# Kernel optimization log

Hardware: AMD Instinct MI355X
Metric: run time of the kernel (lower is better)

Reference implementation:

```python
import jax, jax.numpy as jnp
import numpy as np

H = 512    # hidden size
NF = 512   # num_factor
B, S = 128, 64
D0, D1 = 1536, 2048


def setup_inputs() -> dict:
    key = jax.random.key(0)
    ks = jax.random.split(key, 14)
    stdv = 1.0 / np.sqrt(H)
    u = lambda k, shape: jax.random.uniform(k, shape, jnp.float32, -stdv, stdv)
    return {
        "x0": jax.random.normal(ks[0], (B, S, D0), jnp.float32),  # auxiliary stream (skip_info=1)
        "x1": jax.random.normal(ks[1], (B, S, D1), jnp.float32),  # main encoded stream
        # SVD_Weights for stream 0 (num_gate=2, no individual part) -> weight_fh
        "wa0": u(ks[2], (2 * H, NF)),
        "wb0": jax.random.uniform(ks[3], (NF, 1), jnp.float32, 1 - stdv, 1 + stdv),
        "wc0": u(ks[4], (NF, D0)),
        "b0": u(ks[5], (2 * H,)),
        # SVD_Weights for stream 1 (num_gate=2 shared + individual) -> weight_ih
        "wa1": u(ks[6], (2 * H, NF)),
        "wb1": jax.random.uniform(ks[7], (NF, 1), jnp.float32, 1 - stdv, 1 + stdv),
        "wc1": u(ks[8], (NF, D1)),
        "b1": u(ks[9], (2 * H,)),
        "iw1": u(ks[10], (H, D1)),
        "ib1": u(ks[11], (H,)),
        # GRU hidden-to-hidden params
        "whh": u(ks[12], (3 * H, H)),
        "bhh": u(ks[13], (3 * H,)),
    }


def _svd_weight(wa, wb, wc):
    # tag = [[1.]] (length_tag == 1)  ->  mid = wb @ tag = wb[:, 0]
    # W = wa @ diag(mid) @ wc
    return (wa * wb[:, 0][None, :]) @ wc


def reference(x0, x1, wa0, wb0, wc0, b0, wa1, wb1, wc1, b1, iw1, ib1, whh, bhh):
    bsz = x1.shape[0]
    # get_all_params for stream 1: [2H shared gates; H individual n-gate]
    w_ih = jnp.concatenate([_svd_weight(wa1, wb1, wc1), iw1], axis=0)  # [3H, D1]
    b_ih = jnp.concatenate([b1, ib1], axis=0)                          # [3H]
    # get_shared_params for stream 0: auxiliary gate contributions
    w_fh = _svd_weight(wa0, wb0, wc0)                                  # [2H, D0]

    # Precompute all input-side projections (time-parallel GEMMs)
    gi = jnp.einsum('bsd,gd->bsg', x1, w_ih) + b_ih   # [B,S,3H]
    gf = jnp.einsum('bsd,gd->bsg', x0, w_fh) + b0     # [B,S,2H]
    i_r, i_i, i_n = jnp.split(gi, 3, axis=-1)
    f_r, f_i = jnp.split(gf, 2, axis=-1)

    def step(hx, xs):
        ir, ii, inn, fr, fi = xs
        gh = hx @ whh.T + bhh
        h_r, h_i, h_n = jnp.split(gh, 3, axis=-1)
        r = jax.nn.sigmoid(ir + h_r + fr)
        z = jax.nn.sigmoid(ii + h_i + fi)
        n = jnp.tanh(inn + r * h_n)
        hy = n + z * (hx - n)
        return hy, hy

    xs = tuple(jnp.swapaxes(a, 0, 1) for a in (i_r, i_i, i_n, f_r, f_i))  # time-major
    h0 = jnp.zeros((bsz, H), x1.dtype)
    hT, out = jax.lax.scan(step, h0, xs)
    return jnp.swapaxes(out, 0, 1), hT  # ([B,S,H], [B,H])
```

## Files before the change

### kernel.cpp

```cpp
#include <hip/hip_runtime.h>

#define AS1 __attribute__((address_space(1)))
#define AS3 __attribute__((address_space(3)))

typedef __attribute__((ext_vector_type(8))) short short8;
typedef __attribute__((ext_vector_type(4))) float f32x4;

static __device__ __forceinline__ unsigned short f2bf(float f) {
    unsigned u = __builtin_bit_cast(unsigned, f);
    u += 0x7FFFu + ((u >> 16) & 1u);
    return (unsigned short)(u >> 16);
}


__global__ void cvt_bf16_kernel(const float* __restrict__ in,
                                unsigned short* __restrict__ out, int n8) {
    int i = blockIdx.x * blockDim.x + threadIdx.x;
    int stride = gridDim.x * blockDim.x;
    for (; i < n8; i += stride) {
        const float4* p = (const float4*)in + 2 * (size_t)i;
        float4 a = p[0], b = p[1];
        short8 o;
        o[0] = f2bf(a.x); o[1] = f2bf(a.y); o[2] = f2bf(a.z); o[3] = f2bf(a.w);
        o[4] = f2bf(b.x); o[5] = f2bf(b.y); o[6] = f2bf(b.z); o[7] = f2bf(b.w);
        *(short8*)(out + 8 * (size_t)i) = o;
    }
}

__global__ void wab_kernel(const float* __restrict__ wa, const float* __restrict__ wb,
                           unsigned short* __restrict__ out, int n8) {
    int i = blockIdx.x * blockDim.x + threadIdx.x;
    int stride = gridDim.x * blockDim.x;
    for (; i < n8; i += stride) {
        int base = i * 8;
        int k = base & 511;
        const float4* pa = (const float4*)(wa + base);
        const float4* pb = (const float4*)(wb + k);
        float4 a0 = pa[0], a1 = pa[1], b0 = pb[0], b1 = pb[1];
        short8 o;
        o[0] = f2bf(a0.x * b0.x); o[1] = f2bf(a0.y * b0.y);
        o[2] = f2bf(a0.z * b0.z); o[3] = f2bf(a0.w * b0.w);
        o[4] = f2bf(a1.x * b1.x); o[5] = f2bf(a1.y * b1.y);
        o[6] = f2bf(a1.z * b1.z); o[7] = f2bf(a1.w * b1.w);
        *(short8*)(out + 8 * (size_t)i) = o;
    }
}

__global__ void wcT_kernel(const float* __restrict__ wc,
                           unsigned short* __restrict__ out, int N) {
    int i = blockIdx.x * blockDim.x + threadIdx.x;
    int total = N * 512;
    int stride = gridDim.x * blockDim.x;
    for (; i < total; i += stride) {
        int n = i >> 9, k = i & 511;
        out[i] = f2bf(wc[(size_t)k * N + n]);
    }
}

__global__ void bih_kernel(const float* __restrict__ b1, const float* __restrict__ ib1,
                           float* __restrict__ out) {
    int i = blockIdx.x * blockDim.x + threadIdx.x;
    if (i < 1536) out[i] = (i < 1024) ? b1[i] : ib1[i - 1024];
}

__global__ void scan_init_kernel(unsigned short* __restrict__ hbf,
                                 unsigned* __restrict__ flags) {
    int i = blockIdx.x * blockDim.x + threadIdx.x;
    if (i < 65536) hbf[i] = 0;
    if (i < 128) flags[i] = 0;
}


template <typename OutT, bool BIAS>
__global__ __launch_bounds__(256) void gemm_nt_kernel(
    const unsigned short* __restrict__ A, const unsigned short* __restrict__ B,
    OutT* __restrict__ C, const float* __restrict__ bias, int K, int ldC) {
    __shared__ __align__(16) unsigned short As[128 * 64];
    __shared__ __align__(16) unsigned short Bs[128 * 64];
    const int tid = threadIdx.x;
    const int wave = tid >> 6, lane = tid & 63;
    const long bm = (long)blockIdx.x * 128, bn = (long)blockIdx.y * 128;
    const int wr = (wave >> 1) * 64, wc = (wave & 1) * 64;
    f32x4 acc[4][4] = {};

    const int srow = tid >> 3;
    const int scol = (tid & 7) * 8;
    const unsigned short* Ag = A + bm * K + scol;
    const unsigned short* Bg = B + bn * K + scol;

    for (int kt = 0; kt < K; kt += 64) {
        __syncthreads();
#pragma unroll
        for (int i = 0; i < 4; ++i) {
            __builtin_amdgcn_global_load_lds(
                (const AS1 void*)(Ag + (long)(i * 32 + srow) * K + kt),
                (AS3 void*)(As + i * 2048 + wave * 512), 16, 0, 0);
        }
#pragma unroll
        for (int i = 0; i < 4; ++i) {
            __builtin_amdgcn_global_load_lds(
                (const AS1 void*)(Bg + (long)(i * 32 + srow) * K + kt),
                (AS3 void*)(Bs + i * 2048 + wave * 512), 16, 0, 0);
        }
        __syncthreads();
#pragma unroll
        for (int kk = 0; kk < 2; ++kk) {
            const int ko = kk * 32 + (lane >> 4) * 8;
            short8 af[4], bfr[4];
#pragma unroll
            for (int mi = 0; mi < 4; ++mi)
                af[mi] = *(const short8*)(As + (wr + mi * 16 + (lane & 15)) * 64 + ko);
#pragma unroll
            for (int ni = 0; ni < 4; ++ni)
                bfr[ni] = *(const short8*)(Bs + (wc + ni * 16 + (lane & 15)) * 64 + ko);
#pragma unroll
            for (int mi = 0; mi < 4; ++mi)
#pragma unroll
                for (int ni = 0; ni < 4; ++ni)
                    acc[mi][ni] = __builtin_amdgcn_mfma_f32_16x16x32_bf16(
                        af[mi], bfr[ni], acc[mi][ni], 0, 0, 0);
        }
    }

    const int rbase = (lane >> 4) * 4;
    const int cbase = lane & 15;
#pragma unroll
    for (int mi = 0; mi < 4; ++mi) {
#pragma unroll
        for (int ni = 0; ni < 4; ++ni) {
            long gc = bn + wc + ni * 16 + cbase;
            float bv = BIAS ? bias[gc] : 0.f;
#pragma unroll
            for (int j = 0; j < 4; ++j) {
                long gr = bm + wr + mi * 16 + rbase + j;
                float v = acc[mi][ni][j] + bv;
                if constexpr (sizeof(OutT) == 2)
                    C[gr * ldC + gc] = (OutT)f2bf(v);
                else
                    C[gr * ldC + gc] = v;
            }
        }
    }
}


__global__ __launch_bounds__(256, 1) void gru_scan_kernel(
    unsigned short* __restrict__ hbuf,
    const unsigned short* __restrict__ whh,
    const float* __restrict__ bhh,
    const float* __restrict__ gi, const float* __restrict__ gf,
    float* __restrict__ out, float* __restrict__ hT,
    unsigned* __restrict__ flags) {
    __shared__ __align__(16) unsigned short h_lds[16 * 512];
    __shared__ __align__(16) float gis[48 * 68];
    __shared__ __align__(16) float gfs[32 * 68];

    const int tid = threadIdx.x;
    const int lane = tid & 63;
    const int wv = tid >> 6;
    const int team = blockIdx.x >> 3;
    const int member = blockIdx.x & 7;
    const int r0 = team * 16;
    const int cb = member * 64;
    const int c0 = cb + wv * 16;
    const int lrow = lane & 15;
    const int q = lane >> 4;

    short8 wf[3][16];
#pragma unroll
    for (int g = 0; g < 3; ++g)
#pragma unroll
        for (int kk = 0; kk < 16; ++kk)
            wf[g][kk] = *(const short8*)(whh + (size_t)(g * 512 + c0 + lrow) * 512 + kk * 32 + q * 8);

    const int hc = c0 + lrow;
    const float br = bhh[hc], bz = bhh[512 + hc], bn_ = bhh[1024 + hc];
    const int rb = r0 + q * 4;
    const int lc = wv * 16 + lrow;
    float hprev[4] = {0.f, 0.f, 0.f, 0.f};

    const int chunk_sub = tid >> 4;
    const int u4 = (tid & 15) * 4;
    float4 sl[5];
    auto slab_load = [&](int t) {
#pragma unroll
        for (int k = 0; k < 5; ++k) {
            int chunk = k * 16 + chunk_sub;
            const float* p;
            if (chunk < 48) {
                int bbq = chunk / 3, g = chunk - bbq * 3;
                p = gi + ((size_t)(r0 + bbq) * 64 + t) * 1536 + g * 512 + cb + u4;
            } else {
                int c2 = chunk - 48, bbq = c2 >> 1, g2 = c2 & 1;
                p = gf + ((size_t)(r0 + bbq) * 64 + t) * 1024 + g2 * 512 + cb + u4;
            }
            sl[k] = *(const float4*)p;
        }
    };
    slab_load(0);

    for (int t = 0; t < 64; ++t) {
        if (t > 0 && tid < 64) {
            const unsigned tgt = (unsigned)t;
            for (;;) {
                unsigned v = __hip_atomic_load(&flags[team * 16 + (lane & 7)],
                                               __ATOMIC_RELAXED, __HIP_MEMORY_SCOPE_AGENT);
                if (__all((int)(v >= tgt))) break;
                __builtin_amdgcn_s_sleep(1);
            }
            __builtin_amdgcn_fence(__ATOMIC_ACQUIRE, "agent");
        }
        __syncthreads();

        {
            const unsigned short* hin = hbuf + (t & 1) * 65536;
            const int srow = tid >> 4;
            const unsigned long long* hs =
                (const unsigned long long*)(hin + (size_t)(r0 + srow) * 512);
            unsigned long long hq[8];
#pragma unroll
            for (int k = 0; k < 8; ++k)
                hq[k] = __hip_atomic_load(hs + (tid & 15) + k * 16,
                                          __ATOMIC_RELAXED, __HIP_MEMORY_SCOPE_AGENT);
            char* dst = (char*)h_lds + srow * 1024;
            const int sw = (srow & 7) << 4;
#pragma unroll
            for (int k = 0; k < 8; ++k) {
                int byte = ((tid & 15) + k * 16) * 8;
                *(unsigned long long*)(dst + (byte ^ sw)) = hq[k];
            }
        }
#pragma unroll
        for (int k = 0; k < 5; ++k) {
            int chunk = k * 16 + chunk_sub;
            float* d = (chunk < 48) ? &gis[chunk * 68] : &gfs[(chunk - 48) * 68];
            *(float4*)(d + u4) = sl[k];
        }
        __syncthreads();

        if (t < 63) slab_load(t + 1);

        f32x4 acc0 = {}, acc1 = {}, acc2 = {};
        {
            const char* hl = (const char*)h_lds + lrow * 1024;
            const int sw2 = (lrow & 7) << 4;
#pragma unroll
            for (int kk = 0; kk < 16; ++kk) {
                short8 a = *(const short8*)(hl + ((kk * 64 + q * 16) ^ sw2));
                acc0 = __builtin_amdgcn_mfma_f32_16x16x32_bf16(a, wf[0][kk], acc0, 0, 0, 0);
                acc1 = __builtin_amdgcn_mfma_f32_16x16x32_bf16(a, wf[1][kk], acc1, 0, 0, 0);
                acc2 = __builtin_amdgcn_mfma_f32_16x16x32_bf16(a, wf[2][kk], acc2, 0, 0, 0);
            }
        }

        float hy4[4];
        unsigned short* hout = hbuf + ((t & 1) ^ 1) * 65536;
#pragma unroll
        for (int j = 0; j < 4; ++j) {
            const int bbq = q * 4 + j;
            float ir  = gis[(bbq * 3 + 0) * 68 + lc];
            float ii  = gis[(bbq * 3 + 1) * 68 + lc];
            float inn = gis[(bbq * 3 + 2) * 68 + lc];
            float fr  = gfs[(bbq * 2 + 0) * 68 + lc];
            float fi  = gfs[(bbq * 2 + 1) * 68 + lc];
            float r = 1.f / (1.f + __expf(-(ir + acc0[j] + br + fr)));
            float z = 1.f / (1.f + __expf(-(ii + acc1[j] + bz + fi)));
            float n = tanhf(inn + r * (acc2[j] + bn_));
            float hy = n + z * (hprev[j] - n);
            hprev[j] = hy;
            hy4[j] = hy;
            __hip_atomic_store(hout + (size_t)(rb + j) * 512 + hc,
                               (unsigned short)f2bf(hy),
                               __ATOMIC_RELAXED, __HIP_MEMORY_SCOPE_AGENT);
            __hip_atomic_store(&out[((size_t)(rb + j) * 64 + t) * 512 + hc], hy,
                               __ATOMIC_RELAXED, __HIP_MEMORY_SCOPE_AGENT);
        }

        __syncthreads();
        if (t < 63) {
            if (tid == 0) {
                __builtin_amdgcn_fence(__ATOMIC_RELEASE, "agent");
                __hip_atomic_store(&flags[team * 16 + member], (unsigned)(t + 1),
                                   __ATOMIC_RELAXED, __HIP_MEMORY_SCOPE_AGENT);
            }
        } else {
#pragma unroll
            for (int j = 0; j < 4; ++j)
                __hip_atomic_store(&hT[(size_t)(rb + j) * 512 + hc], hy4[j],
                                   __ATOMIC_RELAXED, __HIP_MEMORY_SCOPE_AGENT);
        }
    }
}


extern "C" void kernel_launch(void* const* d_in, const int* in_sizes, int n_in,
                              void* d_out, int out_size, void* d_ws, size_t ws_size,
                              hipStream_t stream) {
    (void)in_sizes; (void)n_in; (void)out_size; (void)ws_size;

    const float* x0  = (const float*)d_in[0];
    const float* x1  = (const float*)d_in[1];
    const float* wa0 = (const float*)d_in[2];
    const float* wb0 = (const float*)d_in[3];
    const float* wc0 = (const float*)d_in[4];
    const float* b0  = (const float*)d_in[5];
    const float* wa1 = (const float*)d_in[6];
    const float* wb1 = (const float*)d_in[7];
    const float* wc1 = (const float*)d_in[8];
    const float* b1  = (const float*)d_in[9];
    const float* iw1 = (const float*)d_in[10];
    const float* ib1 = (const float*)d_in[11];
    const float* whh = (const float*)d_in[12];
    const float* bhh = (const float*)d_in[13];

    float* out = (float*)d_out;
    float* hT  = out + (size_t)128 * 64 * 512;

    char* w = (char*)d_ws;
    auto alloc = [&](size_t bytes) {
        char* p = w;
        w += (bytes + 255) & ~(size_t)255;
        return p;
    };
    unsigned short* x1bf = (unsigned short*)alloc((size_t)8192 * 2048 * 2);
    unsigned short* x0bf = (unsigned short*)alloc((size_t)8192 * 1536 * 2);
    unsigned short* wih  = (unsigned short*)alloc((size_t)1536 * 2048 * 2);
    unsigned short* wfh  = (unsigned short*)alloc((size_t)1024 * 1536 * 2);
    unsigned short* wab0 = (unsigned short*)alloc((size_t)1024 * 512 * 2);
    unsigned short* wab1 = (unsigned short*)alloc((size_t)1024 * 512 * 2);
    unsigned short* wc0T = (unsigned short*)alloc((size_t)1536 * 512 * 2);
    unsigned short* wc1T = (unsigned short*)alloc((size_t)2048 * 512 * 2);
    unsigned short* whhb = (unsigned short*)alloc((size_t)1536 * 512 * 2);
    float* bih = (float*)alloc(1536 * 4);
    unsigned short* hbf = (unsigned short*)alloc((size_t)2 * 65536 * 2);
    unsigned* flags = (unsigned*)alloc(128 * 4);
    float* gi  = (float*)alloc((size_t)8192 * 1536 * 4);
    float* gf  = (float*)alloc((size_t)8192 * 1024 * 4);

    cvt_bf16_kernel<<<2048, 256, 0, stream>>>(x1, x1bf, (8192 * 2048) / 8);
    cvt_bf16_kernel<<<2048, 256, 0, stream>>>(x0, x0bf, (8192 * 1536) / 8);
    wab_kernel<<<256, 256, 0, stream>>>(wa0, wb0, wab0, (1024 * 512) / 8);
    wab_kernel<<<256, 256, 0, stream>>>(wa1, wb1, wab1, (1024 * 512) / 8);
    wcT_kernel<<<768, 256, 0, stream>>>(wc0, wc0T, 1536);
    wcT_kernel<<<1024, 256, 0, stream>>>(wc1, wc1T, 2048);
    cvt_bf16_kernel<<<384, 256, 0, stream>>>(whh, whhb, (1536 * 512) / 8);
    cvt_bf16_kernel<<<512, 256, 0, stream>>>(iw1, wih + (size_t)1024 * 2048, (512 * 2048) / 8);
    bih_kernel<<<6, 256, 0, stream>>>(b1, ib1, bih);
    scan_init_kernel<<<256, 256, 0, stream>>>(hbf, flags);

    gemm_nt_kernel<unsigned short, false><<<dim3(8, 12), 256, 0, stream>>>(
        wab0, wc0T, wfh, nullptr, 512, 1536);
    gemm_nt_kernel<unsigned short, false><<<dim3(8, 16), 256, 0, stream>>>(
        wab1, wc1T, wih, nullptr, 512, 2048);

    gemm_nt_kernel<float, true><<<dim3(64, 12), 256, 0, stream>>>(
        x1bf, wih, gi, bih, 2048, 1536);
    gemm_nt_kernel<float, true><<<dim3(64, 8), 256, 0, stream>>>(
        x0bf, wfh, gf, b0, 1536, 1024);

    gru_scan_kernel<<<64, 256, 0, stream>>>(hbf, whhb, bhh, gi, gf, out, hT, flags);
}
```

Baseline: 632.0 us.

## Stage GRU outputs in LDS and coalesce hidden and output global stores

Each step's new hidden state and output values now go to LDS first instead of being stored scattered per element to global memory. One wave writes the bf16 hidden state to global with 64-bit atomic stores, then issues the release fence and sets the flag. Waves 2-3 write the previous step's fp32 output from a double-buffered LDS copy while wave 1 spins on the flags. The goal is to shorten the critical path between computing h and publishing it, and to hide output writes under the barrier wait, at the cost of extra LDS and a deferred final flush.

After: 697.1 us. 10.3% more time.

```diff
diff --git a/kernel.cpp b/kernel.cpp
--- a/kernel.cpp
+++ b/kernel.cpp
@@ -5,6 +5,7 @@
 
 typedef __attribute__((ext_vector_type(8))) short short8;
 typedef __attribute__((ext_vector_type(4))) float f32x4;
+typedef unsigned long long u64;
 
 static __device__ __forceinline__ unsigned short f2bf(float f) {
     unsigned u = __builtin_bit_cast(unsigned, f);
@@ -154,6 +155,8 @@
     __shared__ __align__(16) unsigned short h_lds[16 * 512];
     __shared__ __align__(16) float gis[48 * 68];
     __shared__ __align__(16) float gfs[32 * 68];
+    __shared__ __align__(16) unsigned short hy_lds[16 * 64];
+    __shared__ __align__(16) float out_lds[2][16 * 64];
 
     const int tid = threadIdx.x;
     const int lane = tid & 63;
@@ -200,24 +203,37 @@
     slab_load(0);
 
     for (int t = 0; t < 64; ++t) {
-        if (t > 0 && tid < 64) {
-            const unsigned tgt = (unsigned)t;
-            for (;;) {
-                unsigned v = __hip_atomic_load(&flags[team * 16 + (lane & 7)],
-                                               __ATOMIC_RELAXED, __HIP_MEMORY_SCOPE_AGENT);
-                if (__all((int)(v >= tgt))) break;
-                __builtin_amdgcn_s_sleep(1);
-            }
-            __builtin_amdgcn_fence(__ATOMIC_ACQUIRE, "agent");
+        if (t > 0) {
+            if (wv == 1) {
+                const unsigned tgt = (unsigned)t;
+                for (;;) {
+                    unsigned v = __hip_atomic_load(&flags[team * 16 + (lane & 7)],
+                                                   __ATOMIC_RELAXED, __HIP_MEMORY_SCOPE_AGENT);
+                    if (__all((int)(v >= tgt))) break;
+                    __builtin_amdgcn_s_sleep(1);
+                }
+                __builtin_amdgcn_fence(__ATOMIC_ACQUIRE, "agent");
+            } else if (wv >= 2) {
+                const u64* src = (const u64*)out_lds[(t - 1) & 1];
+                const int u = tid - 128;
+#pragma unroll
+                for (int it = 0; it < 4; ++it) {
+                    int idx = it * 128 + u;
+                    int row = idx >> 5;
+                    int c2 = idx & 31;
+                    u64* dst = (u64*)(out + ((size_t)(r0 + row) * 64 + (t - 1)) * 512 + cb);
+                    __hip_atomic_store(dst + c2, src[idx],
+                                       __ATOMIC_RELAXED, __HIP_MEMORY_SCOPE_AGENT);
+                }
+            }
         }
         __syncthreads();
 
         {
             const unsigned short* hin = hbuf + (t & 1) * 65536;
             const int srow = tid >> 4;
-            const unsigned long long* hs =
-                (const unsigned long long*)(hin + (size_t)(r0 + srow) * 512);
-            unsigned long long hq[8];
+            const u64* hs = (const u64*)(hin + (size_t)(r0 + srow) * 512);
+            u64 hq[8];
 #pragma unroll
             for (int k = 0; k < 8; ++k)
                 hq[k] = __hip_atomic_load(hs + (tid & 15) + k * 16,
@@ -227,7 +243,7 @@
 #pragma unroll
             for (int k = 0; k < 8; ++k) {
                 int byte = ((tid & 15) + k * 16) * 8;
-                *(unsigned long long*)(dst + (byte ^ sw)) = hq[k];
+                *(u64*)(dst + (byte ^ sw)) = hq[k];
             }
         }
 #pragma unroll
@@ -253,8 +269,6 @@
             }
         }
 
-        float hy4[4];
-        unsigned short* hout = hbuf + ((t & 1) ^ 1) * 65536;
 #pragma unroll
         for (int j = 0; j < 4; ++j) {
             const int bbq = q * 4 + j;
@@ -268,26 +282,45 @@
             float n = tanhf(inn + r * (acc2[j] + bn_));
             float hy = n + z * (hprev[j] - n);
             hprev[j] = hy;
-            hy4[j] = hy;
-            __hip_atomic_store(hout + (size_t)(rb + j) * 512 + hc,
-                               (unsigned short)f2bf(hy),
-                               __ATOMIC_RELAXED, __HIP_MEMORY_SCOPE_AGENT);
-            __hip_atomic_store(&out[((size_t)(rb + j) * 64 + t) * 512 + hc], hy,
-                               __ATOMIC_RELAXED, __HIP_MEMORY_SCOPE_AGENT);
-        }
-
-        __syncthreads();
+            hy_lds[bbq * 64 + lc] = f2bf(hy);
+            out_lds[t & 1][bbq * 64 + lc] = hy;
+            if (t == 63)
+                __hip_atomic_store(&hT[(size_t)(rb + j) * 512 + hc], hy,
+                                   __ATOMIC_RELAXED, __HIP_MEMORY_SCOPE_AGENT);
+        }
+
+        __syncthreads();
+
         if (t < 63) {
-            if (tid == 0) {
+            if (wv == 0) {
+                unsigned short* hout = hbuf + ((t & 1) ^ 1) * 65536;
+#pragma unroll
+                for (int it = 0; it < 4; ++it) {
+                    int idx = it * 64 + lane;
+                    u64 v = ((const u64*)hy_lds)[idx];
+                    u64* dst = (u64*)(hout + (size_t)(r0 + (idx >> 4)) * 512 + cb);
+                    __hip_atomic_store(dst + (idx & 15), v,
+                                       __ATOMIC_RELAXED, __HIP_MEMORY_SCOPE_AGENT);
+                }
                 __builtin_amdgcn_fence(__ATOMIC_RELEASE, "agent");
-                __hip_atomic_store(&flags[team * 16 + member], (unsigned)(t + 1),
-                                   __ATOMIC_RELAXED, __HIP_MEMORY_SCOPE_AGENT);
+                if (tid == 0)
+                    __hip_atomic_store(&flags[team * 16 + member], (unsigned)(t + 1),
+                                       __ATOMIC_RELAXED, __HIP_MEMORY_SCOPE_AGENT);
             }
         } else {
-#pragma unroll
-            for (int j = 0; j < 4; ++j)
-                __hip_atomic_store(&hT[(size_t)(rb + j) * 512 + hc], hy4[j],
-                                   __ATOMIC_RELAXED, __HIP_MEMORY_SCOPE_AGENT);
+            if (wv >= 2) {
+                const u64* src = (const u64*)out_lds[1];
+                const int u = tid - 128;
+#pragma unroll
+                for (int it = 0; it < 4; ++it) {
+                    int idx = it * 128 + u;
+                    int row = idx >> 5;
+                    int c2 = idx & 31;
+                    u64* dst = (u64*)(out + ((size_t)(r0 + row) * 64 + 63) * 512 + cb);
+                    __hip_atomic_store(dst + c2, src[idx],
+                                       __ATOMIC_RELAXED, __HIP_MEMORY_SCOPE_AGENT);
+                }
+            }
         }
     }
 }
```

## Stage hidden state in LDS and publish with wide stores and release flag

Applied to the files above, without the earlier changes.

The GRU scan kernel now gathers each block's new bf16 hidden values in shared memory and publishes them to the global exchange buffer as one 64-bit atomic store per thread, replacing scattered 16-bit atomic stores. Readers fetch the peer hidden state with 128-bit cache-bypassing loads (sc0 sc1 nt) through inline asm instead of 64-bit atomic loads. The separate fence is replaced by a release-ordered flag store, and the output stores become nontemporal. The aim is to shorten the per-step cross-block exchange on the serial critical path, at the cost of an extra barrier and reliance on the asm cache-bypass bits for correct visibility.

New measurement: 746.2 us. 1.18x slower.

```diff
diff --git a/kernel.cpp b/kernel.cpp
--- a/kernel.cpp
+++ b/kernel.cpp
@@ -5,6 +5,8 @@
 
 typedef __attribute__((ext_vector_type(8))) short short8;
 typedef __attribute__((ext_vector_type(4))) float f32x4;
+typedef __attribute__((ext_vector_type(4))) int int4v;
+typedef unsigned long long u64;
 
 static __device__ __forceinline__ unsigned short f2bf(float f) {
     unsigned u = __builtin_bit_cast(unsigned, f);
@@ -154,6 +156,7 @@
     __shared__ __align__(16) unsigned short h_lds[16 * 512];
     __shared__ __align__(16) float gis[48 * 68];
     __shared__ __align__(16) float gfs[32 * 68];
+    __shared__ __align__(16) unsigned short hy_lds[16 * 64];
 
     const int tid = threadIdx.x;
     const int lane = tid & 63;
@@ -215,19 +218,23 @@
         {
             const unsigned short* hin = hbuf + (t & 1) * 65536;
             const int srow = tid >> 4;
-            const unsigned long long* hs =
-                (const unsigned long long*)(hin + (size_t)(r0 + srow) * 512);
-            unsigned long long hq[8];
-#pragma unroll
-            for (int k = 0; k < 8; ++k)
-                hq[k] = __hip_atomic_load(hs + (tid & 15) + k * 16,
-                                          __ATOMIC_RELAXED, __HIP_MEMORY_SCOPE_AGENT);
+            const int cpos = tid & 15;
+            const char* src = (const char*)(hin + (size_t)(r0 + srow) * 512);
+            int4v hq[4];
+#pragma unroll
+            for (int k = 0; k < 4; ++k) {
+                const void* p = src + (size_t)(cpos + k * 16) * 16;
+                asm volatile("global_load_dwordx4 %0, %1, off sc0 sc1 nt"
+                             : "=v"(hq[k]) : "v"(p) : "memory");
+            }
+            asm volatile("s_waitcnt vmcnt(0)" ::: "memory");
+            __builtin_amdgcn_sched_barrier(0);
             char* dst = (char*)h_lds + srow * 1024;
             const int sw = (srow & 7) << 4;
 #pragma unroll
-            for (int k = 0; k < 8; ++k) {
-                int byte = ((tid & 15) + k * 16) * 8;
-                *(unsigned long long*)(dst + (byte ^ sw)) = hq[k];
+            for (int k = 0; k < 4; ++k) {
+                int byte = (cpos + k * 16) * 16;
+                *(int4v*)(dst + (byte ^ sw)) = hq[k];
             }
         }
 #pragma unroll
@@ -253,8 +260,6 @@
             }
         }
 
-        float hy4[4];
-        unsigned short* hout = hbuf + ((t & 1) ^ 1) * 65536;
 #pragma unroll
         for (int j = 0; j < 4; ++j) {
             const int bbq = q * 4 + j;
@@ -268,26 +273,23 @@
             float n = tanhf(inn + r * (acc2[j] + bn_));
             float hy = n + z * (hprev[j] - n);
             hprev[j] = hy;
-            hy4[j] = hy;
-            __hip_atomic_store(hout + (size_t)(rb + j) * 512 + hc,
-                               (unsigned short)f2bf(hy),
-                               __ATOMIC_RELAXED, __HIP_MEMORY_SCOPE_AGENT);
-            __hip_atomic_store(&out[((size_t)(rb + j) * 64 + t) * 512 + hc], hy,
-                               __ATOMIC_RELAXED, __HIP_MEMORY_SCOPE_AGENT);
-        }
-
-        __syncthreads();
+            hy_lds[bbq * 64 + lc] = f2bf(hy);
+            __builtin_nontemporal_store(hy, &out[((size_t)(rb + j) * 64 + t) * 512 + hc]);
+            if (t == 63)
+                __builtin_nontemporal_store(hy, &hT[(size_t)(rb + j) * 512 + hc]);
+        }
+
+        __syncthreads();
+
         if (t < 63) {
-            if (tid == 0) {
-                __builtin_amdgcn_fence(__ATOMIC_RELEASE, "agent");
+            unsigned short* hout = hbuf + ((t & 1) ^ 1) * 65536;
+            u64 v = ((const u64*)hy_lds)[tid];
+            u64* dst = (u64*)(hout + (size_t)(r0 + (tid >> 4)) * 512 + cb) + (tid & 15);
+            __hip_atomic_store(dst, v, __ATOMIC_RELAXED, __HIP_MEMORY_SCOPE_AGENT);
+            __syncthreads();
+            if (tid == 0)
                 __hip_atomic_store(&flags[team * 16 + member], (unsigned)(t + 1),
-                                   __ATOMIC_RELAXED, __HIP_MEMORY_SCOPE_AGENT);
-            }
-        } else {
-#pragma unroll
-            for (int j = 0; j < 4; ++j)
-                __hip_atomic_store(&hT[(size_t)(rb + j) * 512 + hc], hy4[j],
-                                   __ATOMIC_RELAXED, __HIP_MEMORY_SCOPE_AGENT);
+                                   __ATOMIC_RELEASE, __HIP_MEMORY_SCOPE_AGENT);
         }
     }
 }
```
